# Kernel tuning notes

Hardware: AMD Instinct MI355X
Metric: run time of the kernel (lower is better)

## Reference

```python
import jax, jax.numpy as jnp
import numpy as np

N, DEG, F = 500000, 16, 128
H1, H2, OUT = 256, 256, 128


def setup_inputs() -> dict:
    key = jax.random.key(0)
    ks = jax.random.split(key, 8)
    s = lambda fan_in: 1.0 / np.sqrt(fan_in)
    return {
        "message": jax.random.normal(ks[0], (N, DEG, F), dtype=jnp.float32),
        "features": jax.random.normal(ks[1], (N, F), dtype=jnp.float32),
        "global_features": jax.random.normal(ks[2], (N, F), dtype=jnp.float32),
        "W1": jax.random.normal(ks[3], (3 * F, H1), dtype=jnp.float32) * s(3 * F),
        "b1": jnp.zeros((H1,), dtype=jnp.float32),
        "W2": jax.random.normal(ks[4], (H1, H2), dtype=jnp.float32) * s(H1),
        "b2": jnp.zeros((H2,), dtype=jnp.float32),
        "W3": jax.random.normal(ks[5], (H2, OUT), dtype=jnp.float32) * s(H2),
        "b3": jnp.zeros((OUT,), dtype=jnp.float32),
    }


def reference(message, features, global_features, W1, b1, W2, b2, W3, b3):
    # mailbox sum-aggregate over neighbors: [N, deg, F] -> [N, F]
    agg = jnp.sum(message, axis=1)
    # concat aggregated messages with node + global features: [N, 3F]
    x = jnp.concatenate([agg, features, global_features], axis=1)
    # MLP: Linear+ReLU, Linear+ReLU, Linear
    h = jax.nn.relu(x @ W1 + b1)
    h = jax.nn.relu(h @ W2 + b2)
    out = h @ W3 + b3
    # row-wise L2 (Frobenius over dim=1) normalization
    norm = jnp.linalg.norm(out, axis=1, keepdims=True)
    return out / (norm + 1e-8)
```

## Files before the change

kernel.cpp:

```cpp
#include <hip/hip_runtime.h>


typedef short short8   __attribute__((ext_vector_type(8)));
typedef short short4_t __attribute__((ext_vector_type(4)));
typedef float f32x4    __attribute__((ext_vector_type(4)));

#define SWZ(row, off) ((off) ^ (((row) & 7) << 4))

__device__ __forceinline__ unsigned short f2bf(float f) {
    unsigned int u = __float_as_uint(f);
    u += 0x7fffu + ((u >> 16) & 1u);
    return (unsigned short)(u >> 16);
}

__global__ void prep_weights(const float* __restrict__ W1,
                             const float* __restrict__ W2,
                             const float* __restrict__ W3,
                             short* __restrict__ pw1,
                             short* __restrict__ pw2,
                             short* __restrict__ pw3) {
    int idx = blockIdx.x * 256 + threadIdx.x;
    if (idx < 98304) {
        int j = idx & 7, l = (idx >> 3) & 63, g = idx >> 9;
        int ks = g % 12, tn = g / 12;
        int n = tn * 16 + (l & 15);
        int k = ks * 32 + ((l >> 4) << 3) + j;
        pw1[idx] = (short)f2bf(W1[k * 256 + n]);
    } else if (idx < 98304 + 65536) {
        int e = idx - 98304;
        int j = e & 7, l = (e >> 3) & 63, g = e >> 9;
        int ks = g & 7, tn = g >> 3;
        int n = tn * 16 + (l & 15);
        int k = ks * 32 + ((l >> 4) << 3) + j;
        pw2[e] = (short)f2bf(W2[k * 256 + n]);
    } else if (idx < 98304 + 65536 + 32768) {
        int e = idx - 98304 - 65536;
        int j = e & 7, l = (e >> 3) & 63, g = e >> 9;
        int ks = g & 7, tn = g >> 3;
        int n = tn * 16 + (l & 15);
        int k = ks * 32 + ((l >> 4) << 3) + j;
        pw3[e] = (short)f2bf(W3[k * 128 + n]);
    }
}

__global__ __launch_bounds__(256, 4) void node_net(
    const float* __restrict__ msg,
    const float* __restrict__ feat,
    const float* __restrict__ glob,
    const float* __restrict__ b1v,
    const float* __restrict__ b2v,
    const float* __restrict__ b3v,
    const short* __restrict__ pw1,
    const short* __restrict__ pw2,
    const short* __restrict__ pw3,
    float* __restrict__ out,
    int n_rows)
{
    __shared__ char lds[32768];
    char* regA = lds;
    char* regB = lds + 16384;

    const int tid  = threadIdx.x;
    const int lane = tid & 63;
    const int w    = tid >> 6;
    const int lr   = lane & 15;
    const int lk   = lane >> 4;
    const long long r0 = (long long)blockIdx.x * 32;

    const f32x4 zero4 = {0.f, 0.f, 0.f, 0.f};

    f32x4 acc1[2][4];
    #pragma unroll
    for (int ri = 0; ri < 2; ++ri)
        #pragma unroll
        for (int ci = 0; ci < 4; ++ci) acc1[ri][ci] = zero4;

    #pragma unroll
    for (int p = 0; p < 3; ++p) {
        if (p == 0) {
            #pragma unroll
            for (int pass = 0; pass < 2; ++pass) {
                const int f4 = tid & 31;
                const int rA = (tid >> 5) + pass * 16;
                const int rB = rA + 8;
                const long long rowA = r0 + rA, rowB = r0 + rB;
                f32x4 a = zero4, b = zero4;
                const f32x4* mpA = (const f32x4*)msg + rowA * 512 + f4;
                const f32x4* mpB = (const f32x4*)msg + rowB * 512 + f4;
                if (rowB < n_rows) {
                    #pragma unroll
                    for (int d = 0; d < 16; ++d) { a += mpA[d * 32]; b += mpB[d * 32]; }
                } else if (rowA < n_rows) {
                    #pragma unroll
                    for (int d = 0; d < 16; ++d) { a += mpA[d * 32]; }
                }
                short4_t sa, sb;
                sa[0] = (short)f2bf(a[0]); sa[1] = (short)f2bf(a[1]);
                sa[2] = (short)f2bf(a[2]); sa[3] = (short)f2bf(a[3]);
                sb[0] = (short)f2bf(b[0]); sb[1] = (short)f2bf(b[1]);
                sb[2] = (short)f2bf(b[2]); sb[3] = (short)f2bf(b[3]);
                *(short4_t*)(regB + SWZ(rA, rA * 256 + f4 * 8)) = sa;
                *(short4_t*)(regB + SWZ(rB, rB * 256 + f4 * 8)) = sb;
            }
        } else {
            const f32x4* sp = (const f32x4*)(p == 1 ? feat : glob);
            #pragma unroll
            for (int pass = 0; pass < 4; ++pass) {
                const int f4 = tid & 31;
                const int r  = (tid >> 5) + pass * 8;
                const long long row = r0 + r;
                f32x4 a = zero4;
                if (row < n_rows) a = sp[row * 32 + f4];
                short4_t s4;
                s4[0] = (short)f2bf(a[0]); s4[1] = (short)f2bf(a[1]);
                s4[2] = (short)f2bf(a[2]); s4[3] = (short)f2bf(a[3]);
                *(short4_t*)(regB + SWZ(r, r * 256 + f4 * 8)) = s4;
            }
        }
        __syncthreads();

        #pragma unroll
        for (int s = 0; s < 4; ++s) {
            const int ks = p * 4 + s;
            short8 a[2], b[4];
            #pragma unroll
            for (int ri = 0; ri < 2; ++ri) {
                int row = ri * 16 + lr;
                int off = row * 256 + s * 64 + lk * 16;
                a[ri] = *(const short8*)(regB + SWZ(row, off));
            }
            #pragma unroll
            for (int ci = 0; ci < 4; ++ci) {
                int tn = w * 4 + ci;
                b[ci] = *(const short8*)(pw1 + (((tn * 12 + ks) * 64 + lane) << 3));
            }
            #pragma unroll
            for (int ri = 0; ri < 2; ++ri)
                #pragma unroll
                for (int ci = 0; ci < 4; ++ci)
                    acc1[ri][ci] = __builtin_amdgcn_mfma_f32_16x16x32_bf16(
                        a[ri], b[ci], acc1[ri][ci], 0, 0, 0);
        }
        __syncthreads();
    }

    #pragma unroll
    for (int ci = 0; ci < 4; ++ci) {
        int col = w * 64 + ci * 16 + lr;
        float bias = b1v[col];
        #pragma unroll
        for (int ri = 0; ri < 2; ++ri)
            #pragma unroll
            for (int i = 0; i < 4; ++i) {
                int row = ri * 16 + lk * 4 + i;
                float v = fmaxf(acc1[ri][ci][i] + bias, 0.f);
                int off = row * 512 + col * 2;
                *(short*)(regA + SWZ(row, off)) = (short)f2bf(v);
            }
    }
    __syncthreads();

    f32x4 acc2[2][4];
    #pragma unroll
    for (int ri = 0; ri < 2; ++ri)
        #pragma unroll
        for (int ci = 0; ci < 4; ++ci) acc2[ri][ci] = zero4;

    #pragma unroll
    for (int s = 0; s < 8; ++s) {
        short8 a[2], b[4];
        #pragma unroll
        for (int ri = 0; ri < 2; ++ri) {
            int row = ri * 16 + lr;
            int off = row * 512 + s * 64 + lk * 16;
            a[ri] = *(const short8*)(regA + SWZ(row, off));
        }
        #pragma unroll
        for (int ci = 0; ci < 4; ++ci) {
            int tn = w * 4 + ci;
            b[ci] = *(const short8*)(pw2 + (((tn * 8 + s) * 64 + lane) << 3));
        }
        #pragma unroll
        for (int ri = 0; ri < 2; ++ri)
            #pragma unroll
            for (int ci = 0; ci < 4; ++ci)
                acc2[ri][ci] = __builtin_amdgcn_mfma_f32_16x16x32_bf16(
                    a[ri], b[ci], acc2[ri][ci], 0, 0, 0);
    }

    #pragma unroll
    for (int ci = 0; ci < 4; ++ci) {
        int col = w * 64 + ci * 16 + lr;
        float bias = b2v[col];
        #pragma unroll
        for (int ri = 0; ri < 2; ++ri)
            #pragma unroll
            for (int i = 0; i < 4; ++i) {
                int row = ri * 16 + lk * 4 + i;
                float v = fmaxf(acc2[ri][ci][i] + bias, 0.f);
                int off = row * 512 + col * 2;
                *(short*)(regB + SWZ(row, off)) = (short)f2bf(v);
            }
    }
    __syncthreads();

    f32x4 acc3[2][2];
    #pragma unroll
    for (int ri = 0; ri < 2; ++ri)
        #pragma unroll
        for (int ci = 0; ci < 2; ++ci) acc3[ri][ci] = zero4;

    #pragma unroll
    for (int s = 0; s < 8; ++s) {
        short8 a[2], b[2];
        #pragma unroll
        for (int ri = 0; ri < 2; ++ri) {
            int row = ri * 16 + lr;
            int off = row * 512 + s * 64 + lk * 16;
            a[ri] = *(const short8*)(regB + SWZ(row, off));
        }
        #pragma unroll
        for (int ci = 0; ci < 2; ++ci) {
            int tn = w * 2 + ci;
            b[ci] = *(const short8*)(pw3 + (((tn * 8 + s) * 64 + lane) << 3));
        }
        #pragma unroll
        for (int ri = 0; ri < 2; ++ri)
            #pragma unroll
            for (int ci = 0; ci < 2; ++ci)
                acc3[ri][ci] = __builtin_amdgcn_mfma_f32_16x16x32_bf16(
                    a[ri], b[ci], acc3[ri][ci], 0, 0, 0);
    }

    #pragma unroll
    for (int ci = 0; ci < 2; ++ci) {
        int col = w * 32 + ci * 16 + lr;
        float bias = b3v[col];
        #pragma unroll
        for (int ri = 0; ri < 2; ++ri)
            #pragma unroll
            for (int i = 0; i < 4; ++i) {
                int row = ri * 16 + lk * 4 + i;
                float v = acc3[ri][ci][i] + bias;
                int off = row * 512 + col * 4;
                *(float*)(regA + SWZ(row, off)) = v;
            }
    }
    __syncthreads();

    #pragma unroll
    for (int pass = 0; pass < 4; ++pass) {
        const int r  = (tid >> 5) + pass * 8;
        const int fl = tid & 31;
        int off = r * 512 + fl * 16;
        f32x4 v = *(const f32x4*)(regA + SWZ(r, off));
        float ss = v[0]*v[0] + v[1]*v[1] + v[2]*v[2] + v[3]*v[3];
        ss += __shfl_xor(ss, 1, 32);
        ss += __shfl_xor(ss, 2, 32);
        ss += __shfl_xor(ss, 4, 32);
        ss += __shfl_xor(ss, 8, 32);
        ss += __shfl_xor(ss, 16, 32);
        float inv = 1.f / (sqrtf(ss) + 1e-8f);
        long long row = r0 + r;
        if (row < n_rows) {
            f32x4 o = v * inv;
            ((f32x4*)out)[row * 32 + fl] = o;
        }
    }
}

extern "C" void kernel_launch(void* const* d_in, const int* in_sizes, int n_in,
                              void* d_out, int out_size, void* d_ws, size_t ws_size,
                              hipStream_t stream) {
    const float* msg  = (const float*)d_in[0];
    const float* feat = (const float*)d_in[1];
    const float* glob = (const float*)d_in[2];
    const float* W1   = (const float*)d_in[3];
    const float* b1   = (const float*)d_in[4];
    const float* W2   = (const float*)d_in[5];
    const float* b2   = (const float*)d_in[6];
    const float* W3   = (const float*)d_in[7];
    const float* b3   = (const float*)d_in[8];
    float* out = (float*)d_out;

    const int n_rows = in_sizes[1] / 128;

    short* pw1 = (short*)d_ws;
    short* pw2 = pw1 + 98304;
    short* pw3 = pw2 + 65536;

    hipLaunchKernelGGL(prep_weights, dim3(768), dim3(256), 0, stream,
                       W1, W2, W3, pw1, pw2, pw3);

    const int nblocks = (n_rows + 31) / 32;
    hipLaunchKernelGGL(node_net, dim3(nblocks), dim3(256), 0, stream,
                       msg, feat, glob, b1, b2, b3, pw1, pw2, pw3, out, n_rows);
}
```

Measured before the change: 1.285 ms.

## Split neighbor aggregation into a streaming kernel and prefetch node features

The 16-way message sum moves out of the MLP kernel into a dedicated streaming kernel that writes bf16 aggregates to workspace. The MLP kernel then loads these small aggregates plus feature and global rows, prefetched into registers up front, and runs the three K-chunks of layer 1 using separate LDS regions with fewer barriers. The aim is to stop the large message read from stalling the MFMA kernel, which runs at limited occupancy. The cost is an extra launch and a bf16 aggregate round trip through global memory, and it assumes the workspace is large enough to hold that buffer.

```diff
diff --git a/kernel.cpp b/kernel.cpp
--- a/kernel.cpp
+++ b/kernel.cpp
@@ -43,8 +43,25 @@
     }
 }
 
+__global__ __launch_bounds__(256) void agg_kernel(
+    const float* __restrict__ msg, short* __restrict__ agg, int n_rows)
+{
+    long long t = (long long)blockIdx.x * 256 + threadIdx.x;
+    long long row = t >> 5;
+    int f4 = (int)(t & 31);
+    if (row >= n_rows) return;
+    const f32x4* mp = (const f32x4*)msg + row * 512 + f4;
+    f32x4 s = {0.f, 0.f, 0.f, 0.f};
+    #pragma unroll
+    for (int d = 0; d < 16; ++d) s += mp[d * 32];
+    short4_t s4;
+    s4[0] = (short)f2bf(s[0]); s4[1] = (short)f2bf(s[1]);
+    s4[2] = (short)f2bf(s[2]); s4[3] = (short)f2bf(s[3]);
+    *(short4_t*)(agg + row * 128 + f4 * 4) = s4;
+}
+
 __global__ __launch_bounds__(256, 4) void node_net(
-    const float* __restrict__ msg,
+    const short* __restrict__ aggb,
     const float* __restrict__ feat,
     const float* __restrict__ glob,
     const float* __restrict__ b1v,
@@ -69,6 +86,38 @@
 
     const f32x4 zero4 = {0.f, 0.f, 0.f, 0.f};
 
+    f32x4 fr[4], gr[4];
+    #pragma unroll
+    for (int q = 0; q < 4; ++q) {
+        int r = (tid >> 5) + q * 8;
+        long long row = r0 + r;
+        fr[q] = zero4; gr[q] = zero4;
+        if (row < n_rows) {
+            fr[q] = ((const f32x4*)feat)[row * 32 + (tid & 31)];
+            gr[q] = ((const f32x4*)glob)[row * 32 + (tid & 31)];
+        }
+    }
+
+    #pragma unroll
+    for (int pass = 0; pass < 2; ++pass) {
+        int r = tid >> 3;
+        int c = (tid & 7) + 8 * pass;
+        long long row = r0 + r;
+        short8 v = {0, 0, 0, 0, 0, 0, 0, 0};
+        if (row < n_rows) v = *(const short8*)(aggb + row * 128 + c * 8);
+        *(short8*)(regB + SWZ(r, r * 256 + c * 16)) = v;
+    }
+    __syncthreads();
+
+    #pragma unroll
+    for (int q = 0; q < 4; ++q) {
+        int r = (tid >> 5) + q * 8;
+        short4_t s4;
+        s4[0] = (short)f2bf(fr[q][0]); s4[1] = (short)f2bf(fr[q][1]);
+        s4[2] = (short)f2bf(fr[q][2]); s4[3] = (short)f2bf(fr[q][3]);
+        *(short4_t*)(regA + SWZ(r, r * 256 + (tid & 31) * 8)) = s4;
+    }
+
     f32x4 acc1[2][4];
     #pragma unroll
     for (int ri = 0; ri < 2; ++ri)
@@ -76,72 +125,77 @@
         for (int ci = 0; ci < 4; ++ci) acc1[ri][ci] = zero4;
 
     #pragma unroll
-    for (int p = 0; p < 3; ++p) {
-        if (p == 0) {
-            #pragma unroll
-            for (int pass = 0; pass < 2; ++pass) {
-                const int f4 = tid & 31;
-                const int rA = (tid >> 5) + pass * 16;
-                const int rB = rA + 8;
-                const long long rowA = r0 + rA, rowB = r0 + rB;
-                f32x4 a = zero4, b = zero4;
-                const f32x4* mpA = (const f32x4*)msg + rowA * 512 + f4;
-                const f32x4* mpB = (const f32x4*)msg + rowB * 512 + f4;
-                if (rowB < n_rows) {
-                    #pragma unroll
-                    for (int d = 0; d < 16; ++d) { a += mpA[d * 32]; b += mpB[d * 32]; }
-                } else if (rowA < n_rows) {
-                    #pragma unroll
-                    for (int d = 0; d < 16; ++d) { a += mpA[d * 32]; }
-                }
-                short4_t sa, sb;
-                sa[0] = (short)f2bf(a[0]); sa[1] = (short)f2bf(a[1]);
-                sa[2] = (short)f2bf(a[2]); sa[3] = (short)f2bf(a[3]);
-                sb[0] = (short)f2bf(b[0]); sb[1] = (short)f2bf(b[1]);
-                sb[2] = (short)f2bf(b[2]); sb[3] = (short)f2bf(b[3]);
-                *(short4_t*)(regB + SWZ(rA, rA * 256 + f4 * 8)) = sa;
-                *(short4_t*)(regB + SWZ(rB, rB * 256 + f4 * 8)) = sb;
-            }
-        } else {
-            const f32x4* sp = (const f32x4*)(p == 1 ? feat : glob);
-            #pragma unroll
-            for (int pass = 0; pass < 4; ++pass) {
-                const int f4 = tid & 31;
-                const int r  = (tid >> 5) + pass * 8;
-                const long long row = r0 + r;
-                f32x4 a = zero4;
-                if (row < n_rows) a = sp[row * 32 + f4];
-                short4_t s4;
-                s4[0] = (short)f2bf(a[0]); s4[1] = (short)f2bf(a[1]);
-                s4[2] = (short)f2bf(a[2]); s4[3] = (short)f2bf(a[3]);
-                *(short4_t*)(regB + SWZ(r, r * 256 + f4 * 8)) = s4;
-            }
-        }
-        __syncthreads();
-
-        #pragma unroll
-        for (int s = 0; s < 4; ++s) {
-            const int ks = p * 4 + s;
-            short8 a[2], b[4];
-            #pragma unroll
-            for (int ri = 0; ri < 2; ++ri) {
-                int row = ri * 16 + lr;
-                int off = row * 256 + s * 64 + lk * 16;
-                a[ri] = *(const short8*)(regB + SWZ(row, off));
-            }
-            #pragma unroll
-            for (int ci = 0; ci < 4; ++ci) {
-                int tn = w * 4 + ci;
-                b[ci] = *(const short8*)(pw1 + (((tn * 12 + ks) * 64 + lane) << 3));
-            }
-            #pragma unroll
-            for (int ri = 0; ri < 2; ++ri)
-                #pragma unroll
-                for (int ci = 0; ci < 4; ++ci)
-                    acc1[ri][ci] = __builtin_amdgcn_mfma_f32_16x16x32_bf16(
-                        a[ri], b[ci], acc1[ri][ci], 0, 0, 0);
-        }
-        __syncthreads();
+    for (int s = 0; s < 4; ++s) {
+        short8 a[2], b[4];
+        #pragma unroll
+        for (int ri = 0; ri < 2; ++ri) {
+            int row = ri * 16 + lr;
+            a[ri] = *(const short8*)(regB + SWZ(row, row * 256 + s * 64 + lk * 16));
+        }
+        #pragma unroll
+        for (int ci = 0; ci < 4; ++ci) {
+            int tn = w * 4 + ci;
+            b[ci] = *(const short8*)(pw1 + (((tn * 12 + s) * 64 + lane) << 3));
+        }
+        #pragma unroll
+        for (int ri = 0; ri < 2; ++ri)
+            #pragma unroll
+            for (int ci = 0; ci < 4; ++ci)
+                acc1[ri][ci] = __builtin_amdgcn_mfma_f32_16x16x32_bf16(
+                    a[ri], b[ci], acc1[ri][ci], 0, 0, 0);
+    }
+    __syncthreads();
+
+    #pragma unroll
+    for (int q = 0; q < 4; ++q) {
+        int r = (tid >> 5) + q * 8;
+        short4_t s4;
+        s4[0] = (short)f2bf(gr[q][0]); s4[1] = (short)f2bf(gr[q][1]);
+        s4[2] = (short)f2bf(gr[q][2]); s4[3] = (short)f2bf(gr[q][3]);
+        *(short4_t*)(regB + 8192 + SWZ(r, r * 256 + (tid & 31) * 8)) = s4;
+    }
+
+    #pragma unroll
+    for (int s = 0; s < 4; ++s) {
+        short8 a[2], b[4];
+        #pragma unroll
+        for (int ri = 0; ri < 2; ++ri) {
+            int row = ri * 16 + lr;
+            a[ri] = *(const short8*)(regA + SWZ(row, row * 256 + s * 64 + lk * 16));
+        }
+        #pragma unroll
+        for (int ci = 0; ci < 4; ++ci) {
+            int tn = w * 4 + ci;
+            b[ci] = *(const short8*)(pw1 + (((tn * 12 + 4 + s) * 64 + lane) << 3));
+        }
+        #pragma unroll
+        for (int ri = 0; ri < 2; ++ri)
+            #pragma unroll
+            for (int ci = 0; ci < 4; ++ci)
+                acc1[ri][ci] = __builtin_amdgcn_mfma_f32_16x16x32_bf16(
+                    a[ri], b[ci], acc1[ri][ci], 0, 0, 0);
+    }
+    __syncthreads();
+
+    #pragma unroll
+    for (int s = 0; s < 4; ++s) {
+        short8 a[2], b[4];
+        #pragma unroll
+        for (int ri = 0; ri < 2; ++ri) {
+            int row = ri * 16 + lr;
+            a[ri] = *(const short8*)(regB + 8192 + SWZ(row, row * 256 + s * 64 + lk * 16));
+        }
+        #pragma unroll
+        for (int ci = 0; ci < 4; ++ci) {
+            int tn = w * 4 + ci;
+            b[ci] = *(const short8*)(pw1 + (((tn * 12 + 8 + s) * 64 + lane) << 3));
+        }
+        #pragma unroll
+        for (int ri = 0; ri < 2; ++ri)
+            #pragma unroll
+            for (int ci = 0; ci < 4; ++ci)
+                acc1[ri][ci] = __builtin_amdgcn_mfma_f32_16x16x32_bf16(
+                    a[ri], b[ci], acc1[ri][ci], 0, 0, 0);
     }
 
     #pragma unroll
@@ -154,8 +208,7 @@
             for (int i = 0; i < 4; ++i) {
                 int row = ri * 16 + lk * 4 + i;
                 float v = fmaxf(acc1[ri][ci][i] + bias, 0.f);
-                int off = row * 512 + col * 2;
-                *(short*)(regA + SWZ(row, off)) = (short)f2bf(v);
+                *(short*)(regA + SWZ(row, row * 512 + col * 2)) = (short)f2bf(v);
             }
     }
     __syncthreads();
@@ -172,8 +225,7 @@
         #pragma unroll
         for (int ri = 0; ri < 2; ++ri) {
             int row = ri * 16 + lr;
-            int off = row * 512 + s * 64 + lk * 16;
-            a[ri] = *(const short8*)(regA + SWZ(row, off));
+            a[ri] = *(const short8*)(regA + SWZ(row, row * 512 + s * 64 + lk * 16));
         }
         #pragma unroll
         for (int ci = 0; ci < 4; ++ci) {
@@ -198,8 +250,7 @@
             for (int i = 0; i < 4; ++i) {
                 int row = ri * 16 + lk * 4 + i;
                 float v = fmaxf(acc2[ri][ci][i] + bias, 0.f);
-                int off = row * 512 + col * 2;
-                *(short*)(regB + SWZ(row, off)) = (short)f2bf(v);
+                *(short*)(regB + SWZ(row, row * 512 + col * 2)) = (short)f2bf(v);
             }
     }
     __syncthreads();
@@ -216,8 +267,7 @@
         #pragma unroll
         for (int ri = 0; ri < 2; ++ri) {
             int row = ri * 16 + lr;
-            int off = row * 512 + s * 64 + lk * 16;
-            a[ri] = *(const short8*)(regB + SWZ(row, off));
+            a[ri] = *(const short8*)(regB + SWZ(row, row * 512 + s * 64 + lk * 16));
         }
         #pragma unroll
         for (int ci = 0; ci < 2; ++ci) {
@@ -242,8 +292,7 @@
             for (int i = 0; i < 4; ++i) {
                 int row = ri * 16 + lk * 4 + i;
                 float v = acc3[ri][ci][i] + bias;
-                int off = row * 512 + col * 4;
-                *(float*)(regA + SWZ(row, off)) = v;
+                *(float*)(regA + SWZ(row, row * 512 + col * 4)) = v;
             }
     }
     __syncthreads();
@@ -252,8 +301,7 @@
     for (int pass = 0; pass < 4; ++pass) {
         const int r  = (tid >> 5) + pass * 8;
         const int fl = tid & 31;
-        int off = r * 512 + fl * 16;
-        f32x4 v = *(const f32x4*)(regA + SWZ(r, off));
+        f32x4 v = *(const f32x4*)(regA + SWZ(r, r * 512 + fl * 16));
         float ss = v[0]*v[0] + v[1]*v[1] + v[2]*v[2] + v[3]*v[3];
         ss += __shfl_xor(ss, 1, 32);
         ss += __shfl_xor(ss, 2, 32);
@@ -285,14 +333,20 @@
 
     const int n_rows = in_sizes[1] / 128;
 
-    short* pw1 = (short*)d_ws;
-    short* pw2 = pw1 + 98304;
-    short* pw3 = pw2 + 65536;
+    short* pw1  = (short*)d_ws;
+    short* pw2  = pw1 + 98304;
+    short* pw3  = pw2 + 65536;
+    short* aggb = pw3 + 32768;
 
     hipLaunchKernelGGL(prep_weights, dim3(768), dim3(256), 0, stream,
                        W1, W2, W3, pw1, pw2, pw3);
 
+    const long long athreads = (long long)n_rows * 32;
+    const int ablocks = (int)((athreads + 255) / 256);
+    hipLaunchKernelGGL(agg_kernel, dim3(ablocks), dim3(256), 0, stream,
+                       msg, aggb, n_rows);
+
     const int nblocks = (n_rows + 31) / 32;
     hipLaunchKernelGGL(node_net, dim3(nblocks), dim3(256), 0, stream,
-                       msg, feat, glob, b1, b2, b3, pw1, pw2, pw3, out, n_rows);
-}
+                       aggb, feat, glob, b1, b2, b3, pw1, pw2, pw3, out, n_rows);
+}
```

New measurement: 1.327 ms. +3.2%, slower.
